# Optimization experiments

Hardware: AMD Instinct MI355X
Metric: run time of the kernel (lower is better)

Reference implementation:

```python
import jax, jax.numpy as jnp
import numpy as np

K = 32            # number of stocks to select (init kwarg k)
TEMP = 1.0        # initial_temperature, no annealing applied
EPS = 1e-10
MASK_SUB = 10000.0


def setup_inputs() -> dict:
    key = jax.random.key(0)
    k1, k2 = jax.random.split(key)
    scores = jax.random.normal(k1, (4096, 8192), dtype=jnp.float32)
    u = jax.random.uniform(k2, (4096, 8192), dtype=jnp.float32)
    return {"scores": scores, "u": u}


def reference(scores, u):
    # gumbel noise exactly as torch: -log(-log(rand + eps) + eps)
    gumbel = -jnp.log(-jnp.log(u + EPS) + EPS)
    perturbed = (scores + gumbel) / TEMP

    # iterative soft top-k: k rounds of softmax + suppress selected mass
    def step(carry, _):
        soft_mask, remaining = carry
        s = jax.nn.softmax(remaining, axis=-1)
        return (soft_mask + s, remaining - s * MASK_SUB), None

    (soft_mask, _), _ = jax.lax.scan(
        step, (jnp.zeros_like(scores), perturbed), None, length=K)

    # hard top-k mask from raw scores
    _, idx = jax.lax.top_k(scores, K)                      # (B, K)
    B = scores.shape[0]
    hard_mask = jnp.zeros_like(scores).at[
        jnp.arange(B)[:, None], idx].set(1.0)

    # straight-through: forward == hard_mask, backward through soft_mask
    return hard_mask - jax.lax.stop_gradient(soft_mask) + soft_mask
```

## Files before the change

### kernel.cpp

```cpp
#include <hip/hip_runtime.h>


constexpr int ROWS  = 4096;
constexpr int COLS  = 8192;
constexpr int TPB   = 256;
constexpr int WAVES = TPB / 64;
constexpr int CPL   = COLS / 64 / 4;
constexpr int KSEL  = 32;
constexpr int CAPW  = 256;
constexpr int BMW   = COLS / 32;

__device__ __forceinline__ unsigned f2key(float f) {
    unsigned b = __float_as_uint(f);
    return (b & 0x80000000u) ? ~b : (b | 0x80000000u);
}

__global__ __launch_bounds__(TPB, 4) void topk_mask_kernel(
        const float* __restrict__ scores, float* __restrict__ out) {
    const int tid  = threadIdx.x;
    const int wv   = tid >> 6;
    const int lane = tid & 63;
    const int row  = blockIdx.x * WAVES + wv;
    const size_t base = (size_t)row * COLS;
    const float4* __restrict__ src = reinterpret_cast<const float4*>(scores + base);
    float4*       __restrict__ dst = reinterpret_cast<float4*>(out + base);

    __shared__ __align__(16) unsigned long long skey[WAVES][CAPW];
    __shared__ __align__(16) unsigned           bmsh[WAVES][BMW];
    unsigned long long* sk  = skey[wv];
    unsigned*           bmw = bmsh[wv];

    reinterpret_cast<uint4*>(bmw)[lane] = make_uint4(0u, 0u, 0u, 0u);

    const unsigned long long ltm = (1ull << lane) - 1ull;

    unsigned cnt = 0;
    for (int attempt = 0; ; ++attempt) {
        const float T = (attempt == 0) ? 2.3f
                      : (attempt == 1) ? 1.9f
                      : (attempt == 2) ? 0.0f : -3.0e38f;
        cnt = 0;
#pragma unroll
        for (int s = 0; s < CAPW / 64; ++s) sk[lane + 64 * s] = 0ull;

#pragma unroll 8
        for (int t = 0; t < CPL; ++t) {
            const float4 v = src[lane + 64 * t];
            const float f[4] = {v.x, v.y, v.z, v.w};
#pragma unroll
            for (int c = 0; c < 4; ++c) {
                const bool pr = f[c] > T;
                const unsigned long long m = __ballot(pr);
                if (m) {
                    if (pr) {
                        const unsigned pos = cnt + (unsigned)__popcll(m & ltm);
                        if (pos < CAPW) {
                            const unsigned idx = 4u * (unsigned)(lane + 64 * t) + c;
                            sk[pos] = ((unsigned long long)f2key(f[c]) << 13)
                                      | (unsigned long long)(8191u - idx);
                        }
                    }
                    cnt += (unsigned)__popcll(m);
                }
            }
        }
        if (cnt >= (unsigned)KSEL || attempt >= 3) break;
    }
    const unsigned C = cnt < (unsigned)CAPW ? cnt : (unsigned)CAPW;

    {
        const ulonglong2* sk2 = reinterpret_cast<const ulonglong2*>(sk);
        const unsigned NP = (C + 1u) >> 1;
        const unsigned NS = (C + 63u) >> 6;
        for (unsigned s = 0; s < NS; ++s) {
            const unsigned long long kq = sk[lane + 64u * s];
            unsigned r = 0;
            for (unsigned p = 0; p < NP; ++p) {
                const ulonglong2 kk = sk2[p];
                r += (kk.x > kq) + (kk.y > kq);
            }
            if (r < (unsigned)KSEL && kq != 0ull) {
                const unsigned idx = 8191u - (unsigned)(kq & 0x1FFFull);
                atomicOr(&bmw[idx >> 5], 1u << (idx & 31u));
            }
        }
    }

    const unsigned sh = 4u * (unsigned)(lane & 7);
#pragma unroll 8
    for (int t = 0; t < CPL; ++t) {
        const unsigned w = bmw[(lane >> 3) + 8 * t];
        float4 o;
        o.x = ((w >> (sh + 0)) & 1u) ? 1.0f : 0.0f;
        o.y = ((w >> (sh + 1)) & 1u) ? 1.0f : 0.0f;
        o.z = ((w >> (sh + 2)) & 1u) ? 1.0f : 0.0f;
        o.w = ((w >> (sh + 3)) & 1u) ? 1.0f : 0.0f;
        dst[lane + 64 * t] = o;
    }
}

extern "C" void kernel_launch(void* const* d_in, const int* in_sizes, int n_in,
                              void* d_out, int out_size, void* d_ws, size_t ws_size,
                              hipStream_t stream) {
    const float* scores = (const float*)d_in[0];
    float* out = (float*)d_out;
    topk_mask_kernel<<<dim3(ROWS / WAVES), dim3(TPB), 0, stream>>>(scores, out);
}
```

Before: 283.3 us.

## Split top-k into bitmap kernel and separate mask-expand kernel via workspace

Splits the fused kernel in two. The first kernel selects the top-k per row and writes a compact per-row bitmap to workspace. The second kernel expands that bitmap into the float output with one block per row. The selection loop also batches eight float4 loads before the ballot processing to expose more memory-level parallelism. The split separates the read-heavy and write-heavy phases, at the cost of an extra launch and a small workspace round trip. If no workspace is provided, the code falls back to the original fused kernel.

```diff
diff --git a/kernel.cpp b/kernel.cpp
--- a/kernel.cpp
+++ b/kernel.cpp
@@ -9,10 +9,115 @@
 constexpr int KSEL  = 32;
 constexpr int CAPW  = 256;
 constexpr int BMW   = COLS / 32;
+constexpr size_t WS_NEED = (size_t)ROWS * BMW * sizeof(unsigned);
 
 __device__ __forceinline__ unsigned f2key(float f) {
     unsigned b = __float_as_uint(f);
     return (b & 0x80000000u) ? ~b : (b | 0x80000000u);
+}
+
+__global__ __launch_bounds__(TPB, 4) void topk_bitmap_kernel(
+        const float* __restrict__ scores, unsigned* __restrict__ ws_bm) {
+    const int tid  = threadIdx.x;
+    const int wv   = tid >> 6;
+    const int lane = tid & 63;
+    const int row  = blockIdx.x * WAVES + wv;
+    const size_t base = (size_t)row * COLS;
+    const float4* __restrict__ src = reinterpret_cast<const float4*>(scores + base);
+
+    __shared__ __align__(16) unsigned long long skey[WAVES][CAPW];
+    __shared__ __align__(16) unsigned           bmsh[WAVES][BMW];
+    unsigned long long* sk  = skey[wv];
+    unsigned*           bmw = bmsh[wv];
+
+    reinterpret_cast<uint4*>(bmw)[lane] = make_uint4(0u, 0u, 0u, 0u);
+
+    const unsigned long long ltm = (1ull << lane) - 1ull;
+
+    unsigned cnt = 0;
+    for (int attempt = 0; ; ++attempt) {
+        const float T = (attempt == 0) ? 2.3f
+                      : (attempt == 1) ? 1.9f
+                      : (attempt == 2) ? 0.0f : -3.0e38f;
+        cnt = 0;
+#pragma unroll
+        for (int s = 0; s < CAPW / 64; ++s) sk[lane + 64 * s] = 0ull;
+
+#pragma unroll
+        for (int g = 0; g < CPL / 8; ++g) {
+            float4 bb[8];
+#pragma unroll
+            for (int j = 0; j < 8; ++j)
+                bb[j] = src[lane + 64 * (8 * g + j)];
+#pragma unroll
+            for (int j = 0; j < 8; ++j) {
+                const int t = 8 * g + j;
+                const float f[4] = {bb[j].x, bb[j].y, bb[j].z, bb[j].w};
+#pragma unroll
+                for (int c = 0; c < 4; ++c) {
+                    const bool pr = f[c] > T;
+                    const unsigned long long m = __ballot(pr);
+                    if (m) {
+                        if (pr) {
+                            const unsigned pos = cnt + (unsigned)__popcll(m & ltm);
+                            if (pos < CAPW) {
+                                const unsigned idx = 4u * (unsigned)(lane + 64 * t) + c;
+                                sk[pos] = ((unsigned long long)f2key(f[c]) << 13)
+                                          | (unsigned long long)(8191u - idx);
+                            }
+                        }
+                        cnt += (unsigned)__popcll(m);
+                    }
+                }
+            }
+        }
+        if (cnt >= (unsigned)KSEL || attempt >= 3) break;
+    }
+    const unsigned C = cnt < (unsigned)CAPW ? cnt : (unsigned)CAPW;
+
+    {
+        const ulonglong2* sk2 = reinterpret_cast<const ulonglong2*>(sk);
+        const unsigned NP = (C + 1u) >> 1;
+        const unsigned NS = (C + 63u) >> 6;
+        for (unsigned s = 0; s < NS; ++s) {
+            const unsigned long long kq = sk[lane + 64u * s];
+            unsigned r = 0;
+            for (unsigned p = 0; p < NP; ++p) {
+                const ulonglong2 kk = sk2[p];
+                r += (kk.x > kq) + (kk.y > kq);
+            }
+            if (r < (unsigned)KSEL && kq != 0ull) {
+                const unsigned idx = 8191u - (unsigned)(kq & 0x1FFFull);
+                atomicOr(&bmw[idx >> 5], 1u << (idx & 31u));
+            }
+        }
+    }
+
+    reinterpret_cast<uint4*>(ws_bm + (size_t)row * BMW)[lane] =
+        reinterpret_cast<const uint4*>(bmw)[lane];
+}
+
+__global__ __launch_bounds__(TPB) void expand_kernel(
+        const unsigned* __restrict__ ws_bm, float* __restrict__ out) {
+    const int tid = threadIdx.x;
+    const int row = blockIdx.x;
+    const unsigned* __restrict__ bmr = ws_bm + (size_t)row * BMW;
+    float4* __restrict__ dst = reinterpret_cast<float4*>(out + (size_t)row * COLS);
+
+    unsigned w[8];
+#pragma unroll
+    for (int j = 0; j < 8; ++j) w[j] = bmr[(tid >> 3) + 32 * j];
+
+    const unsigned sh = 4u * (unsigned)(tid & 7);
+#pragma unroll
+    for (int j = 0; j < 8; ++j) {
+        float4 o;
+        o.x = ((w[j] >> (sh + 0)) & 1u) ? 1.0f : 0.0f;
+        o.y = ((w[j] >> (sh + 1)) & 1u) ? 1.0f : 0.0f;
+        o.z = ((w[j] >> (sh + 2)) & 1u) ? 1.0f : 0.0f;
+        o.w = ((w[j] >> (sh + 3)) & 1u) ? 1.0f : 0.0f;
+        dst[tid + j * TPB] = o;
+    }
 }
 
 __global__ __launch_bounds__(TPB, 4) void topk_mask_kernel(
@@ -31,7 +136,6 @@
     unsigned*           bmw = bmsh[wv];
 
     reinterpret_cast<uint4*>(bmw)[lane] = make_uint4(0u, 0u, 0u, 0u);
-
     const unsigned long long ltm = (1ull << lane) - 1ull;
 
     unsigned cnt = 0;
@@ -42,7 +146,6 @@
         cnt = 0;
 #pragma unroll
         for (int s = 0; s < CAPW / 64; ++s) sk[lane + 64 * s] = 0ull;
-
 #pragma unroll 8
         for (int t = 0; t < CPL; ++t) {
             const float4 v = src[lane + 64 * t];
@@ -104,5 +207,11 @@
                               hipStream_t stream) {
     const float* scores = (const float*)d_in[0];
     float* out = (float*)d_out;
-    topk_mask_kernel<<<dim3(ROWS / WAVES), dim3(TPB), 0, stream>>>(scores, out);
-}
+    if (d_ws != nullptr && ws_size >= WS_NEED) {
+        unsigned* bm = (unsigned*)d_ws;
+        topk_bitmap_kernel<<<dim3(ROWS / WAVES), dim3(TPB), 0, stream>>>(scores, bm);
+        expand_kernel<<<dim3(ROWS), dim3(TPB), 0, stream>>>(bm, out);
+    } else {
+        topk_mask_kernel<<<dim3(ROWS / WAVES), dim3(TPB), 0, stream>>>(scores, out);
+    }
+}
```

Result: slower. 490.1 us (+73.0%).
